# Optimization experiments

Measured on AMD Instinct MI355X. Metric: run time of the kernel, lower is better.

## Reference

```python
import jax, jax.numpy as jnp
import numpy as np

N = 1024        # nodes
E = 524288      # directed edges
FE_IN, FE = 2, 64   # edge feat in / mid
FC = 128        # candidate (node) feat
L = 3           # EGAT conv layers
NEG_SLOPE = 0.2 # DGL leaky_relu default


def setup_inputs() -> dict:
    key = jax.random.key(0)
    ks = jax.random.split(key, 12)
    s = 0.05
    return {
        "node_feature": jax.random.normal(ks[0], (N, FC), jnp.float32),
        "edge_feature": jax.random.normal(ks[1], (E, FE_IN), jnp.float32),
        "src": jax.random.randint(ks[2], (E,), 0, N, dtype=jnp.int32),
        "dst": jax.random.randint(ks[3], (E,), 0, N, dtype=jnp.int32),
        # input edge linear (bias=True)
        "W_in": jax.random.normal(ks[4], (FE_IN, FE), jnp.float32) * s,
        "b_in": jnp.zeros((FE,), jnp.float32),
        # per-layer EGATConv params (num_heads=1)
        "W_ni": jax.random.normal(ks[5], (L, FC, FE), jnp.float32) * s,
        "W_nj": jax.random.normal(ks[6], (L, FC, FE), jnp.float32) * s,
        "W_fij": jax.random.normal(ks[7], (L, FE, FE), jnp.float32) * s,
        "W_node": jax.random.normal(ks[8], (L, FC, FC), jnp.float32) * s,
        "attn": jax.random.normal(ks[9], (L, FE), jnp.float32) * s,
        "bias_node": jnp.zeros((L, FC), jnp.float32),
    }


def _edge_softmax(e, dst):
    # softmax of edge logits e[E] over incoming edges of each dst node
    m = jax.ops.segment_max(e, dst, num_segments=N)
    ex = jnp.exp(e - m[dst])
    z = jax.ops.segment_sum(ex, dst, num_segments=N)
    return ex / z[dst]


def reference(node_feature, edge_feature, src, dst, W_in, b_in,
              W_ni, W_nj, W_fij, W_node, attn, bias_node):
    node = node_feature                       # [N, FC]
    ef = edge_feature @ W_in + b_in           # [E, FE]
    for l in range(L):
        f_ni = node @ W_ni[l]                 # [N, FE]
        f_nj = node @ W_nj[l]                 # [N, FE]
        # edge messages: gather src/dst projections + edge projection
        f_out = jax.nn.leaky_relu(f_ni[src] + f_nj[dst] + ef @ W_fij[l],
                                  NEG_SLOPE)  # [E, FE]
        e = jnp.einsum('ef,f->e', f_out, attn[l])   # [E]
        a = _edge_softmax(e, dst)                    # [E]
        h = node @ W_node[l] + bias_node[l]          # [N, FC]
        new_node = jax.ops.segment_sum(a[:, None] * h[src], dst,
                                       num_segments=N)  # [N, FC]
        # residual fusion (use_residual=True, num_heads=1 so squeeze is a no-op)
        node = node + new_node
        ef = ef + f_out
    return node
```

## Files before the change

### kernel.cpp

```cpp
#include <hip/hip_runtime.h>

#define N_NODES 1024
#define E_EDGES 524288
#define FE 64
#define FC 128
#define NLAYERS 3

typedef unsigned short u16;
typedef __attribute__((ext_vector_type(8))) short bf16x8;
typedef __attribute__((ext_vector_type(4))) float f32x4;
typedef __attribute__((ext_vector_type(8))) unsigned short u16x8;

__device__ __forceinline__ float bf2f(u16 u) {
    return __uint_as_float(((unsigned)u) << 16);
}
__device__ __forceinline__ u16 f2bf(float f) {
    unsigned x = __float_as_uint(f);
    return (u16)((x + 0x7FFFu + ((x >> 16) & 1u)) >> 16);
}

__global__ __launch_bounds__(256) void setup_kernel(
    const float* __restrict__ node_feature, const float* __restrict__ Wfij,
    u16* __restrict__ Wt,
    const float* __restrict__ Wni, const float* __restrict__ Wnj,
    const float* __restrict__ Wnode, const float* __restrict__ bias,
    u16* __restrict__ fni, u16* __restrict__ fnj,
    float* __restrict__ h, float* __restrict__ S, float* __restrict__ nodeA)
{
    __shared__ float row[FC];
    const int d = blockIdx.x;
    const int t = threadIdx.x;

    reinterpret_cast<float4*>(S + (size_t)d * N_NODES)[t] = make_float4(0.f, 0.f, 0.f, 0.f);

    if (t < FC) {
        const float v = node_feature[d * FC + t];
        nodeA[d * FC + t] = v;
        row[t] = v;
    }
    if (d < (NLAYERS * FE * FE) / 256) {
        const int i = d * 256 + t;
        const int l = i >> 12, rem = i & 4095;
        const int n = rem >> 6, k = rem & 63;
        Wt[(size_t)l * 4096 + n * 64 + k] = f2bf(Wfij[(size_t)l * 4096 + k * 64 + n]);
    }
    __syncthreads();

    if (t < 64) {
        float a = 0.f;
        #pragma unroll 8
        for (int k = 0; k < FC; k++) a = fmaf(row[k], Wni[k * FE + t], a);
        fni[d * FE + t] = f2bf(a);
    } else if (t < 128) {
        const int f = t - 64;
        float a = 0.f;
        #pragma unroll 8
        for (int k = 0; k < FC; k++) a = fmaf(row[k], Wnj[k * FE + f], a);
        fnj[d * FE + f] = f2bf(a);
    } else {
        const int c = t - 128;
        float a = bias[c];
        #pragma unroll 8
        for (int k = 0; k < FC; k++) a = fmaf(row[k], Wnode[k * FC + c], a);
        h[d * FC + c] = a;
    }
}

template <bool FIRST, bool WRITE_EF>
__global__ void edge_mfma_kernel(
    u16* __restrict__ ef,
    const float* __restrict__ x,
    const float* __restrict__ Win,
    const float* __restrict__ bin,
    const u16* __restrict__ Wt,
    const u16* __restrict__ fni, const u16* __restrict__ fnj,
    const int* __restrict__ src, const int* __restrict__ dst,
    const float* __restrict__ attn,
    float* __restrict__ S)
{
    __shared__ __align__(16) u16 stage[4][32][72];
    __shared__ __align__(16) u16 fol[WRITE_EF ? 4 : 1][16][72];

    const int lane = threadIdx.x & 63;
    const int wid  = threadIdx.x >> 6;
    const int l15  = lane & 15;
    const int grp  = lane >> 4;
    const int wbase = blockIdx.x * 64 + wid * 16;

    #pragma unroll
    for (int it = 0; it < 4; it++) {
        const int ridx = it * 8 + (lane >> 3);
        const int e = wbase + (ridx & 15);
        const int c8 = (lane & 7) * 8;
        const u16* rowp = (ridx < 16) ? (fni + (size_t)src[e] * FE)
                                      : (fnj + (size_t)dst[e] * FE);
        *reinterpret_cast<u16x8*>(&stage[wid][ridx][c8]) =
            *reinterpret_cast<const u16x8*>(rowp + c8);
    }

    bf16x8 afr0, afr1;
    if constexpr (FIRST) {
        const float2 xx = *reinterpret_cast<const float2*>(x + 2 * (size_t)(wbase + l15));
        #pragma unroll
        for (int half = 0; half < 2; half++) {
            const int c0 = half * 32 + grp * 8;
            const float4 wA0 = *reinterpret_cast<const float4*>(Win + c0);
            const float4 wA1 = *reinterpret_cast<const float4*>(Win + c0 + 4);
            const float4 wB0 = *reinterpret_cast<const float4*>(Win + FE + c0);
            const float4 wB1 = *reinterpret_cast<const float4*>(Win + FE + c0 + 4);
            const float4 b0  = *reinterpret_cast<const float4*>(bin + c0);
            const float4 b1  = *reinterpret_cast<const float4*>(bin + c0 + 4);
            bf16x8 fr;
            fr[0] = (short)f2bf(fmaf(xx.x, wA0.x, fmaf(xx.y, wB0.x, b0.x)));
            fr[1] = (short)f2bf(fmaf(xx.x, wA0.y, fmaf(xx.y, wB0.y, b0.y)));
            fr[2] = (short)f2bf(fmaf(xx.x, wA0.z, fmaf(xx.y, wB0.z, b0.z)));
            fr[3] = (short)f2bf(fmaf(xx.x, wA0.w, fmaf(xx.y, wB0.w, b0.w)));
            fr[4] = (short)f2bf(fmaf(xx.x, wA1.x, fmaf(xx.y, wB1.x, b1.x)));
            fr[5] = (short)f2bf(fmaf(xx.x, wA1.y, fmaf(xx.y, wB1.y, b1.y)));
            fr[6] = (short)f2bf(fmaf(xx.x, wA1.z, fmaf(xx.y, wB1.z, b1.z)));
            fr[7] = (short)f2bf(fmaf(xx.x, wA1.w, fmaf(xx.y, wB1.w, b1.w)));
            if (half == 0) afr0 = fr; else afr1 = fr;
        }
    } else {
        const size_t arow = (size_t)(wbase + l15) * FE;
        afr0 = *reinterpret_cast<const bf16x8*>(ef + arow + grp * 8);
        afr1 = *reinterpret_cast<const bf16x8*>(ef + arow + 32 + grp * 8);
    }

    bf16x8 bfr[2][4];
    #pragma unroll
    for (int ks = 0; ks < 2; ks++)
        #pragma unroll
        for (int nt = 0; nt < 4; nt++)
            bfr[ks][nt] = *reinterpret_cast<const bf16x8*>(
                Wt + (size_t)(nt * 16 + l15) * 64 + ks * 32 + grp * 8);

    f32x4 acc[4];
    #pragma unroll
    for (int nt = 0; nt < 4; nt++) {
        acc[nt] = (f32x4){0.f, 0.f, 0.f, 0.f};
        acc[nt] = __builtin_amdgcn_mfma_f32_16x16x32_bf16(afr0, bfr[0][nt], acc[nt], 0, 0, 0);
        acc[nt] = __builtin_amdgcn_mfma_f32_16x16x32_bf16(afr1, bfr[1][nt], acc[nt], 0, 0, 0);
    }

    float an[4];
    #pragma unroll
    for (int nt = 0; nt < 4; nt++) an[nt] = attn[nt * 16 + l15];

    __builtin_amdgcn_wave_barrier();

    float logit[4] = {0.f, 0.f, 0.f, 0.f};
    #pragma unroll
    for (int nt = 0; nt < 4; nt++) {
        const int n = nt * 16 + l15;
        #pragma unroll
        for (int r = 0; r < 4; r++) {
            const int row = grp * 4 + r;
            float v = acc[nt][r] + bf2f(stage[wid][row][n])
                                 + bf2f(stage[wid][16 + row][n]);
            v = v > 0.f ? v : 0.2f * v;
            logit[r] = fmaf(v, an[nt], logit[r]);
            if constexpr (WRITE_EF) fol[wid][row][n] = f2bf(v);
        }
    }

    #pragma unroll
    for (int r = 0; r < 4; r++) {
        float t = logit[r];
        t += __shfl_xor(t, 1, 16);
        t += __shfl_xor(t, 2, 16);
        t += __shfl_xor(t, 4, 16);
        t += __shfl_xor(t, 8, 16);
        if (l15 == 0) {
            const int e = wbase + grp * 4 + r;
            atomicAdd(S + (size_t)dst[e] * N_NODES + src[e], expf(t));
        }
    }

    if constexpr (WRITE_EF) {
        __builtin_amdgcn_wave_barrier();
        const u16x8 fo0 = *reinterpret_cast<const u16x8*>(&fol[wid][l15][grp * 8]);
        const u16x8 fo1 = *reinterpret_cast<const u16x8*>(&fol[wid][l15][32 + grp * 8]);
        u16x8 o0, o1;
        #pragma unroll
        for (int j = 0; j < 8; j++) {
            o0[j] = f2bf(bf2f((u16)afr0[j]) + bf2f(fo0[j]));
            o1[j] = f2bf(bf2f((u16)afr1[j]) + bf2f(fo1[j]));
        }
        u16* gp = ef + (size_t)(wbase + l15) * FE;
        *reinterpret_cast<u16x8*>(gp + grp * 8) = o0;
        *reinterpret_cast<u16x8*>(gp + 32 + grp * 8) = o1;
    }
}

template <bool LAST>
__global__ __launch_bounds__(256) void spmm_kernel(
    float* __restrict__ S, const float* __restrict__ h,
    const float* __restrict__ nin, float* __restrict__ nout,
    const float* __restrict__ Wni, const float* __restrict__ Wnj,
    const float* __restrict__ Wnode, const float* __restrict__ bias,
    u16* __restrict__ fni, u16* __restrict__ fnj, float* __restrict__ hnext)
{
    __shared__ float red[256];
    __shared__ float rs[2];
    __shared__ float row[FC];
    const int d = blockIdx.x;
    const int t = threadIdx.x;
    const int c = t & 127;
    const int half = t >> 7;
    const float* Srow = S + (size_t)d * N_NODES + half * 512;
    const float* hp = h + (size_t)half * 512 * FC;
    float acc = 0.f, rsum = 0.f;
    #pragma unroll 8
    for (int n = 0; n < 512; n++) {
        const float s = Srow[n];
        rsum += s;
        acc = fmaf(s, hp[n * FC + c], acc);
    }
    red[t] = acc;
    if (c == 0) rs[half] = rsum;
    __syncthreads();

    if constexpr (!LAST) {
        reinterpret_cast<float4*>(S + (size_t)d * N_NODES)[t] = make_float4(0.f, 0.f, 0.f, 0.f);
    }
    if (half == 0) {
        const float v = nin[d * FC + c] + (red[c] + red[128 + c]) / (rs[0] + rs[1]);
        nout[d * FC + c] = v;
        if constexpr (!LAST) row[c] = v;
    }

    if constexpr (!LAST) {
        __syncthreads();
        if (t < 64) {
            float a = 0.f;
            #pragma unroll 8
            for (int k = 0; k < FC; k++) a = fmaf(row[k], Wni[k * FE + t], a);
            fni[d * FE + t] = f2bf(a);
        } else if (t < 128) {
            const int f = t - 64;
            float a = 0.f;
            #pragma unroll 8
            for (int k = 0; k < FC; k++) a = fmaf(row[k], Wnj[k * FE + f], a);
            fnj[d * FE + f] = f2bf(a);
        } else {
            const int cc = t - 128;
            float a = bias[cc];
            #pragma unroll 8
            for (int k = 0; k < FC; k++) a = fmaf(row[k], Wnode[k * FC + cc], a);
            hnext[d * FC + cc] = a;
        }
    }
}

extern "C" void kernel_launch(void* const* d_in, const int* in_sizes, int n_in,
                              void* d_out, int out_size, void* d_ws, size_t ws_size,
                              hipStream_t stream)
{
    const float* node_feature = (const float*)d_in[0];
    const float* edge_feature = (const float*)d_in[1];
    const int*   src          = (const int*)d_in[2];
    const int*   dst          = (const int*)d_in[3];
    const float* W_in         = (const float*)d_in[4];
    const float* b_in         = (const float*)d_in[5];
    const float* W_ni         = (const float*)d_in[6];
    const float* W_nj         = (const float*)d_in[7];
    const float* W_fij        = (const float*)d_in[8];
    const float* W_node       = (const float*)d_in[9];
    const float* attn         = (const float*)d_in[10];
    const float* bias_node    = (const float*)d_in[11];
    float* out = (float*)d_out;

    char* ws = (char*)d_ws;
    size_t off = 0;
    auto alloc = [&](size_t bytes) -> void* {
        void* pp = ws + off;
        off += (bytes + 255) & ~(size_t)255;
        return pp;
    };
    u16*   ef    = (u16*)alloc((size_t)E_EDGES * FE * sizeof(u16));
    u16*   fni   = (u16*)alloc(N_NODES * FE * sizeof(u16));
    u16*   fnj   = (u16*)alloc(N_NODES * FE * sizeof(u16));
    float* h0    = (float*)alloc(N_NODES * FC * sizeof(float));
    float* h1    = (float*)alloc(N_NODES * FC * sizeof(float));
    float* S     = (float*)alloc((size_t)N_NODES * N_NODES * sizeof(float));
    float* nodeA = (float*)alloc(N_NODES * FC * sizeof(float));
    u16*   Wt    = (u16*)alloc((size_t)NLAYERS * FE * FE * sizeof(u16));
    float* hbuf[2] = {h0, h1};

    setup_kernel<<<N_NODES, 256, 0, stream>>>(
        node_feature, W_fij, Wt, W_ni, W_nj, W_node, bias_node,
        fni, fnj, h0, S, nodeA);

    for (int l = 0; l < NLAYERS; l++) {
        float* hl = hbuf[l & 1];
        float* hn = hbuf[(l + 1) & 1];

        if (l == 0) {
            edge_mfma_kernel<true, true><<<E_EDGES / 64, 256, 0, stream>>>(
                ef, edge_feature, W_in, b_in, Wt + (size_t)l * FE * FE,
                fni, fnj, src, dst, attn + (size_t)l * FE, S);
        } else if (l == NLAYERS - 1) {
            edge_mfma_kernel<false, false><<<E_EDGES / 64, 256, 0, stream>>>(
                ef, nullptr, nullptr, nullptr, Wt + (size_t)l * FE * FE,
                fni, fnj, src, dst, attn + (size_t)l * FE, S);
        } else {
            edge_mfma_kernel<false, true><<<E_EDGES / 64, 256, 0, stream>>>(
                ef, nullptr, nullptr, nullptr, Wt + (size_t)l * FE * FE,
                fni, fnj, src, dst, attn + (size_t)l * FE, S);
        }

        if (l == NLAYERS - 1) {
            spmm_kernel<true><<<N_NODES, 256, 0, stream>>>(
                S, hl, nodeA, out,
                nullptr, nullptr, nullptr, nullptr, nullptr, nullptr, nullptr);
        } else {
            const int ln = l + 1;
            spmm_kernel<false><<<N_NODES, 256, 0, stream>>>(
                S, hl, nodeA, nodeA,
                W_ni + (size_t)ln * FC * FE, W_nj + (size_t)ln * FC * FE,
                W_node + (size_t)ln * FC * FC, bias_node + (size_t)ln * FC,
                fni, fnj, hn);
        }
    }
}
```

Before: 285.4 us.

## Transpose edge MFMA so each lane owns one edge, dropping LDS staging

The MFMA operands are swapped so the output tile is laid out as features by edges, and each lane now holds whole columns for a single edge. The src/dst projection gathers then go straight to registers instead of through shared-memory staging. Logit reduction shrinks to two cross-group shuffles with one atomic per edge, and the residual edge-feature update is written directly without the LDS round trip. In exchange the gathers become 8-byte loads per lane rather than 16-byte coalesced rows. The non-first layers also re-read the old edge features from global memory for the residual.

Result: slower. 380.9 us (+33.4%).

```diff
diff --git a/kernel.cpp b/kernel.cpp
--- a/kernel.cpp
+++ b/kernel.cpp
@@ -10,6 +10,7 @@
 typedef __attribute__((ext_vector_type(8))) short bf16x8;
 typedef __attribute__((ext_vector_type(4))) float f32x4;
 typedef __attribute__((ext_vector_type(8))) unsigned short u16x8;
+typedef __attribute__((ext_vector_type(4))) unsigned short u16x4;
 
 __device__ __forceinline__ float bf2f(u16 u) {
     return __uint_as_float(((unsigned)u) << 16);
@@ -78,29 +79,19 @@
     const float* __restrict__ attn,
     float* __restrict__ S)
 {
-    __shared__ __align__(16) u16 stage[4][32][72];
-    __shared__ __align__(16) u16 fol[WRITE_EF ? 4 : 1][16][72];
-
     const int lane = threadIdx.x & 63;
     const int wid  = threadIdx.x >> 6;
     const int l15  = lane & 15;
     const int grp  = lane >> 4;
-    const int wbase = blockIdx.x * 64 + wid * 16;
-
-    #pragma unroll
-    for (int it = 0; it < 4; it++) {
-        const int ridx = it * 8 + (lane >> 3);
-        const int e = wbase + (ridx & 15);
-        const int c8 = (lane & 7) * 8;
-        const u16* rowp = (ridx < 16) ? (fni + (size_t)src[e] * FE)
-                                      : (fnj + (size_t)dst[e] * FE);
-        *reinterpret_cast<u16x8*>(&stage[wid][ridx][c8]) =
-            *reinterpret_cast<const u16x8*>(rowp + c8);
-    }
-
-    bf16x8 afr0, afr1;
+    const int el   = blockIdx.x * 64 + wid * 16 + l15;
+
+    const int se = src[el];
+    const int de = dst[el];
+
+    bf16x8 efr0, efr1;
+    float2 xx;
     if constexpr (FIRST) {
-        const float2 xx = *reinterpret_cast<const float2*>(x + 2 * (size_t)(wbase + l15));
+        xx = *reinterpret_cast<const float2*>(x + 2 * (size_t)el);
         #pragma unroll
         for (int half = 0; half < 2; half++) {
             const int c0 = half * 32 + grp * 8;
@@ -119,77 +110,84 @@
             fr[5] = (short)f2bf(fmaf(xx.x, wA1.y, fmaf(xx.y, wB1.y, b1.y)));
             fr[6] = (short)f2bf(fmaf(xx.x, wA1.z, fmaf(xx.y, wB1.z, b1.z)));
             fr[7] = (short)f2bf(fmaf(xx.x, wA1.w, fmaf(xx.y, wB1.w, b1.w)));
-            if (half == 0) afr0 = fr; else afr1 = fr;
+            if (half == 0) efr0 = fr; else efr1 = fr;
         }
     } else {
-        const size_t arow = (size_t)(wbase + l15) * FE;
-        afr0 = *reinterpret_cast<const bf16x8*>(ef + arow + grp * 8);
-        afr1 = *reinterpret_cast<const bf16x8*>(ef + arow + 32 + grp * 8);
-    }
-
-    bf16x8 bfr[2][4];
+        const size_t arow = (size_t)el * FE;
+        efr0 = *reinterpret_cast<const bf16x8*>(ef + arow + grp * 8);
+        efr1 = *reinterpret_cast<const bf16x8*>(ef + arow + 32 + grp * 8);
+    }
+
+    bf16x8 wfr[2][4];
     #pragma unroll
     for (int ks = 0; ks < 2; ks++)
         #pragma unroll
         for (int nt = 0; nt < 4; nt++)
-            bfr[ks][nt] = *reinterpret_cast<const bf16x8*>(
+            wfr[ks][nt] = *reinterpret_cast<const bf16x8*>(
                 Wt + (size_t)(nt * 16 + l15) * 64 + ks * 32 + grp * 8);
+
+    u16x4 gi[4], gj[4];
+    f32x4 av[4];
+    #pragma unroll
+    for (int nt = 0; nt < 4; nt++) {
+        const int c0 = nt * 16 + grp * 4;
+        gi[nt] = *reinterpret_cast<const u16x4*>(fni + (size_t)se * FE + c0);
+        gj[nt] = *reinterpret_cast<const u16x4*>(fnj + (size_t)de * FE + c0);
+        av[nt] = *reinterpret_cast<const f32x4*>(attn + c0);
+    }
 
     f32x4 acc[4];
     #pragma unroll
     for (int nt = 0; nt < 4; nt++) {
         acc[nt] = (f32x4){0.f, 0.f, 0.f, 0.f};
-        acc[nt] = __builtin_amdgcn_mfma_f32_16x16x32_bf16(afr0, bfr[0][nt], acc[nt], 0, 0, 0);
-        acc[nt] = __builtin_amdgcn_mfma_f32_16x16x32_bf16(afr1, bfr[1][nt], acc[nt], 0, 0, 0);
-    }
-
-    float an[4];
-    #pragma unroll
-    for (int nt = 0; nt < 4; nt++) an[nt] = attn[nt * 16 + l15];
-
-    __builtin_amdgcn_wave_barrier();
-
-    float logit[4] = {0.f, 0.f, 0.f, 0.f};
+        acc[nt] = __builtin_amdgcn_mfma_f32_16x16x32_bf16(wfr[0][nt], efr0, acc[nt], 0, 0, 0);
+        acc[nt] = __builtin_amdgcn_mfma_f32_16x16x32_bf16(wfr[1][nt], efr1, acc[nt], 0, 0, 0);
+    }
+
+    float vv[4][4];
+    float logit = 0.f;
     #pragma unroll
     for (int nt = 0; nt < 4; nt++) {
-        const int n = nt * 16 + l15;
         #pragma unroll
         for (int r = 0; r < 4; r++) {
-            const int row = grp * 4 + r;
-            float v = acc[nt][r] + bf2f(stage[wid][row][n])
-                                 + bf2f(stage[wid][16 + row][n]);
+            float v = acc[nt][r] + bf2f(gi[nt][r]) + bf2f(gj[nt][r]);
             v = v > 0.f ? v : 0.2f * v;
-            logit[r] = fmaf(v, an[nt], logit[r]);
-            if constexpr (WRITE_EF) fol[wid][row][n] = f2bf(v);
-        }
-    }
-
-    #pragma unroll
-    for (int r = 0; r < 4; r++) {
-        float t = logit[r];
-        t += __shfl_xor(t, 1, 16);
-        t += __shfl_xor(t, 2, 16);
-        t += __shfl_xor(t, 4, 16);
-        t += __shfl_xor(t, 8, 16);
-        if (l15 == 0) {
-            const int e = wbase + grp * 4 + r;
-            atomicAdd(S + (size_t)dst[e] * N_NODES + src[e], expf(t));
-        }
+            vv[nt][r] = v;
+            logit = fmaf(v, av[nt][r], logit);
+        }
+    }
+
+    logit += __shfl_xor(logit, 16, 64);
+    logit += __shfl_xor(logit, 32, 64);
+    const float pv = expf(logit);
+    if (grp == 0) {
+        atomicAdd(S + (size_t)de * N_NODES + se, pv);
     }
 
     if constexpr (WRITE_EF) {
-        __builtin_amdgcn_wave_barrier();
-        const u16x8 fo0 = *reinterpret_cast<const u16x8*>(&fol[wid][l15][grp * 8]);
-        const u16x8 fo1 = *reinterpret_cast<const u16x8*>(&fol[wid][l15][32 + grp * 8]);
-        u16x8 o0, o1;
         #pragma unroll
-        for (int j = 0; j < 8; j++) {
-            o0[j] = f2bf(bf2f((u16)afr0[j]) + bf2f(fo0[j]));
-            o1[j] = f2bf(bf2f((u16)afr1[j]) + bf2f(fo1[j]));
-        }
-        u16* gp = ef + (size_t)(wbase + l15) * FE;
-        *reinterpret_cast<u16x8*>(gp + grp * 8) = o0;
-        *reinterpret_cast<u16x8*>(gp + 32 + grp * 8) = o1;
+        for (int nt = 0; nt < 4; nt++) {
+            const int c0 = nt * 16 + grp * 4;
+            u16* gp = ef + (size_t)el * FE + c0;
+            f32x4 oldv;
+            if constexpr (FIRST) {
+                const float4 w0 = *reinterpret_cast<const float4*>(Win + c0);
+                const float4 w1 = *reinterpret_cast<const float4*>(Win + FE + c0);
+                const float4 bb = *reinterpret_cast<const float4*>(bin + c0);
+                oldv[0] = fmaf(xx.x, w0.x, fmaf(xx.y, w1.x, bb.x));
+                oldv[1] = fmaf(xx.x, w0.y, fmaf(xx.y, w1.y, bb.y));
+                oldv[2] = fmaf(xx.x, w0.z, fmaf(xx.y, w1.z, bb.z));
+                oldv[3] = fmaf(xx.x, w0.w, fmaf(xx.y, w1.w, bb.w));
+            } else {
+                const u16x4 ov = *reinterpret_cast<const u16x4*>(gp);
+                oldv[0] = bf2f(ov[0]); oldv[1] = bf2f(ov[1]);
+                oldv[2] = bf2f(ov[2]); oldv[3] = bf2f(ov[3]);
+            }
+            u16x4 o;
+            #pragma unroll
+            for (int r = 0; r < 4; r++) o[r] = f2bf(oldv[r] + vv[nt][r]);
+            *reinterpret_cast<u16x4*>(gp) = o;
+        }
     }
 }
 
```
